# Kernel optimization log

Hardware: AMD Instinct MI355X
Metric: run time of the kernel (lower is better)

The kernel has to match this reference:

```python
import jax, jax.numpy as jnp
import numpy as np

N, C1, C2 = 1024, 384, 128
H, SQK, SV, PQK, PV, OUT = 12, 16, 16, 4, 8, 384
EPS = 1e-8
DOUT = H*SV + 3*H*PV + H*PV + H*C2  # 2112


def setup_inputs():
    key = jax.random.key(0)
    ks = jax.random.split(key, 10)
    inputs_1d = jax.random.normal(ks[0], (N, C1), jnp.float32)
    inputs_2d = jax.random.normal(ks[1], (N, N, C2), jnp.float32)
    mask = jnp.ones((N, 1), jnp.float32)
    # random valid rotations from unit quaternions
    quat = jax.random.normal(ks[2], (N, 4), jnp.float32)
    quat = quat / jnp.linalg.norm(quat, axis=-1, keepdims=True)
    w, x, y, z = quat[:, 0], quat[:, 1], quat[:, 2], quat[:, 3]
    rot = jnp.stack([
        jnp.stack([1 - 2*(y*y + z*z), 2*(x*y - w*z), 2*(x*z + w*y)], -1),
        jnp.stack([2*(x*y + w*z), 1 - 2*(x*x + z*z), 2*(y*z - w*x)], -1),
        jnp.stack([2*(x*z - w*y), 2*(y*z + w*x), 1 - 2*(x*x + y*y)], -1)], -2)
    trans = 10.0 * jax.random.normal(ks[3], (N, 3), jnp.float32)
    s1 = 1.0 / np.sqrt(C1)
    wq = jax.random.normal(ks[4], (C1, H*SQK), jnp.float32) * s1
    bq = jnp.zeros((H*SQK,), jnp.float32)
    wkv = jax.random.normal(ks[5], (C1, H*(SQK + SV)), jnp.float32) * s1
    bkv = jnp.zeros((H*(SQK + SV),), jnp.float32)
    wqp = jax.random.normal(ks[6], (C1, H*3*PQK), jnp.float32) * s1
    bqp = jnp.zeros((H*3*PQK,), jnp.float32)
    wkvp = jax.random.normal(ks[7], (C1, H*3*(PQK + PV)), jnp.float32) * s1
    bkvp = jnp.zeros((H*3*(PQK + PV),), jnp.float32)
    w2d = jax.random.normal(ks[8], (C2, H), jnp.float32) / np.sqrt(C2)
    b2d = jnp.zeros((H,), jnp.float32)
    tpw = jnp.full((H,), np.log(np.e - 1.0), jnp.float32)  # softplus(tpw)=1 at init
    wo = jax.random.normal(ks[9], (DOUT, OUT), jnp.float32) / np.sqrt(DOUT)
    bo = jnp.zeros((OUT,), jnp.float32)
    return dict(inputs_1d=inputs_1d, inputs_2d=inputs_2d, mask=mask, rot=rot, trans=trans,
                wq=wq, bq=bq, wkv=wkv, bkv=bkv, wqp=wqp, bqp=bqp, wkvp=wkvp, bkvp=bkvp,
                w2d=w2d, b2d=b2d, tpw=tpw, wo=wo, bo=bo)


def _ipa(inputs_1d, inputs_2d, mask, rot, trans, wq, bq, wkv, bkv, wqp, bqp,
         wkvp, bkvp, w2d, b2d, tpw, wo, bo):
    n = inputs_1d.shape[0]
    # scalar q/k/v
    q_scalar = (inputs_1d @ wq + bq).reshape(n, H, SQK)
    kv_scalar = (inputs_1d @ wkv + bkv).reshape(n, H, SQK + SV)
    k_scalar, v_scalar = kv_scalar[..., :SQK], kv_scalar[..., SQK:]
    # point q/k/v: local frame -> global frame, x_g = R x_l + t
    q_pl = (inputs_1d @ wqp + bqp).reshape(n, 3, H*PQK)
    q_pg = jnp.einsum('nac,nck->nak', rot, q_pl) + trans[:, :, None]
    q_pt = q_pg.reshape(n, 3, H, PQK).transpose(1, 2, 0, 3)        # (3,H,N,PQK)
    kv_pl = (inputs_1d @ wkvp + bkvp).reshape(n, 3, H*(PQK + PV))
    kv_pg = jnp.einsum('nac,nck->nak', rot, kv_pl) + trans[:, :, None]
    kv_pt = kv_pg.reshape(n, 3, H, PQK + PV).transpose(1, 2, 0, 3)  # (3,H,N,PQK+PV)
    k_pt, v_pt = kv_pt[..., :PQK], kv_pt[..., PQK:]
    # logit weights (3 logit terms)
    scalar_w = np.sqrt(1.0 / (3.0 * SQK))
    point_w = np.sqrt(1.0 / (3.0 * PQK * 9.0 / 2.0)) * jax.nn.softplus(tpw)  # (H,)
    # squared-distance term, expanded to avoid a (3,H,N,N,P) intermediate
    sq = jnp.sum(q_pt * q_pt, axis=(0, 3))                         # (H,N)
    sk = jnp.sum(k_pt * k_pt, axis=(0, 3))                         # (H,N)
    qk = jnp.einsum('chnp,chmp->hnm', q_pt, k_pt)
    dist2 = sq[:, :, None] + sk[:, None, :] - 2.0 * qk             # (H,N,N)
    attn_qk_point = -0.5 * point_w[:, None, None] * dist2
    attn_qk_scalar = jnp.einsum('nhs,mhs->hnm', scalar_w * q_scalar, k_scalar)
    att2d = jnp.transpose(inputs_2d @ w2d + b2d, (2, 0, 1))        # (H,N,N)
    logits = attn_qk_scalar + attn_qk_point + np.sqrt(1.0 / 3.0) * att2d
    mask_2d = mask * jnp.swapaxes(mask, -1, -2)                    # (N,N)
    logits = logits - 1e5 * (1.0 - mask_2d)
    attn = jax.nn.softmax(logits, axis=-1)                         # (H,N,N)
    # aggregate scalar, point and pair outputs with the same weights
    res_scalar = jnp.einsum('hnm,mhs->nhs', attn, v_scalar).reshape(n, H*SV)
    res_pg = jnp.einsum('hnm,chmp->cnhp', attn, v_pt).reshape(3, n, H*PV)
    res_pl = jnp.einsum('nca,cnk->ank', rot, res_pg - trans.T[:, :, None])  # R^T(g-t)
    pt_norm = jnp.sqrt(EPS + jnp.sum(res_pl * res_pl, axis=0))     # (N,H*PV)
    res_2d = jnp.einsum('hnm,nmc->nhc', attn, inputs_2d).reshape(n, H*C2)
    final = jnp.concatenate([res_scalar, res_pl[0], res_pl[1], res_pl[2], pt_norm, res_2d], axis=-1)
    return final @ wo + bo


def reference(inputs_1d, inputs_2d, mask, rot, trans, wq, bq, wkv, bkv, wqp, bqp,
              wkvp, bkvp, w2d, b2d, tpw, wo, bo):
    return _ipa(inputs_1d, inputs_2d, mask, rot, trans, wq, bq, wkv, bkv, wqp, bqp,
                wkvp, bkvp, w2d, b2d, tpw, wo, bo)
```

## Files before the change

kernel.cpp:

```cpp
#include <hip/hip_runtime.h>
#include <math.h>

#define NN_ 1024
#define DOUT_ 2112
#define NOUT_ 384

using f16x8_t = __attribute__((ext_vector_type(8))) _Float16;
using f32x4_t = __attribute__((ext_vector_type(4))) float;

__global__ __launch_bounds__(256) void k_gemm1(
    const float* __restrict__ in1,
    const float* __restrict__ wq, const float* __restrict__ bq,
    const float* __restrict__ wkv, const float* __restrict__ bkv,
    const float* __restrict__ wqp, const float* __restrict__ bqp,
    const float* __restrict__ wkvp, const float* __restrict__ bkvp,
    float* __restrict__ yraw)
{
    __shared__ float a_l[64 * 36];
    __shared__ float b_l[32 * 68];
    const int t = threadIdx.x;
    const int m0 = blockIdx.x * 64, j0 = blockIdx.y * 64;
    const int tx = t & 15, ty = t >> 4;
    float acc[4][4] = {};
    for (int k0 = 0; k0 < 384; k0 += 32) {
        #pragma unroll
        for (int e = 0; e < 2; ++e) {
            int idx = t + 256 * e;
            int r = idx >> 3, c4 = (idx & 7) * 4;
            *(float4*)&a_l[r * 36 + c4] = *(const float4*)&in1[(size_t)(m0 + r) * 384 + k0 + c4];
        }
        #pragma unroll
        for (int e = 0; e < 2; ++e) {
            int idx = t + 256 * e;
            int r = idx >> 4, c4 = (idx & 15) * 4;
            int j = j0 + c4;
            const float* w; int ncol, jj;
            if (j < 192)      { w = wq;   ncol = 192; jj = j; }
            else if (j < 576) { w = wkv;  ncol = 384; jj = j - 192; }
            else if (j < 720) { w = wqp;  ncol = 144; jj = j - 576; }
            else              { w = wkvp; ncol = 432; jj = j - 720; }
            *(float4*)&b_l[r * 68 + c4] = *(const float4*)&w[(size_t)(k0 + r) * ncol + jj];
        }
        __syncthreads();
        #pragma unroll 8
        for (int k = 0; k < 32; ++k) {
            float4 bv = *(const float4*)&b_l[k * 68 + tx * 4];
            #pragma unroll
            for (int i = 0; i < 4; ++i) {
                float av = a_l[(ty * 4 + i) * 36 + k];
                acc[i][0] += av * bv.x; acc[i][1] += av * bv.y;
                acc[i][2] += av * bv.z; acc[i][3] += av * bv.w;
            }
        }
        __syncthreads();
    }
    int j = j0 + tx * 4;
    float4 bias;
    {
        const float* b; int jj;
        if (j < 192)      { b = bq;   jj = j; }
        else if (j < 576) { b = bkv;  jj = j - 192; }
        else if (j < 720) { b = bqp;  jj = j - 576; }
        else              { b = bkvp; jj = j - 720; }
        bias = *(const float4*)&b[jj];
    }
    #pragma unroll
    for (int i = 0; i < 4; ++i) {
        float4 o;
        o.x = acc[i][0] + bias.x; o.y = acc[i][1] + bias.y;
        o.z = acc[i][2] + bias.z; o.w = acc[i][3] + bias.w;
        *(float4*)&yraw[(size_t)(m0 + ty * 4 + i) * 1152 + j] = o;
    }
}

__global__ __launch_bounds__(256) void k_rot(
    const float* __restrict__ yraw, const float* __restrict__ rotm, const float* __restrict__ trans,
    float* __restrict__ qp_arr, float* __restrict__ kpackT4, _Float16* __restrict__ vT,
    float* __restrict__ sq_arr, float* __restrict__ skT)
{
    __shared__ float rt_l[4][12];
    const int t = threadIdx.x;
    const int n0 = blockIdx.x * 4;
    if (t < 48) {
        int n_ = t / 12, i = t % 12;
        rt_l[n_][i] = (i < 9) ? rotm[(n0 + n_) * 9 + i] : trans[(n0 + n_) * 3 + (i - 9)];
    }
    __syncthreads();
    const int n_ = t >> 6, l = t & 63;
    const int n = n0 + n_;
    const float* y = yraw + (size_t)n * 1152;
    const float* R = rt_l[n_];
    #pragma unroll
    for (int jj = 0; jj < 9; ++jj) {
        int o = l + 64 * jj;
        if (o < 144) {
            int a = o / 48, kk = o % 48;
            float v = R[9 + a] + R[a*3+0] * y[576 + kk] + R[a*3+1] * y[576 + 48 + kk] + R[a*3+2] * y[576 + 96 + kk];
            qp_arr[(size_t)n * 144 + o] = v;
        } else if (o < 288) {
            int o2 = o - 144;
            int a = o2 / 48, r2 = o2 % 48;
            int kk = (r2 >> 2) * 12 + (r2 & 3);
            float v = R[9 + a] + R[a*3+0] * y[720 + kk] + R[a*3+1] * y[720 + 144 + kk] + R[a*3+2] * y[720 + 288 + kk];
            int j = 192 + o2;
            kpackT4[(size_t)(j >> 2) * 4096 + 4 * n + (j & 3)] = v;
        } else {
            int o3 = o - 288;
            int a = o3 / 96, r2 = o3 % 96;
            int kk = (r2 >> 3) * 12 + 4 + (r2 & 7);
            float v = R[9 + a] + R[a*3+0] * y[720 + kk] + R[a*3+1] * y[720 + 144 + kk] + R[a*3+2] * y[720 + 288 + kk];
            vT[(size_t)(192 + o3) * 1024 + n] = (_Float16)v;
        }
    }
    #pragma unroll
    for (int jj = 0; jj < 3; ++jj) {
        int o = l + 64 * jj;
        int h = o >> 4, r2 = o & 15;
        kpackT4[(size_t)(o >> 2) * 4096 + 4 * n + (o & 3)] = y[192 + h * 32 + r2];
        vT[(size_t)o * 1024 + n] = (_Float16)y[192 + h * 32 + 16 + r2];
    }
    if (l < 32) vT[(size_t)(480 + l) * 1024 + n] = (_Float16)0.f;
    if (l < 24) {
        int which = l / 12, h = l % 12;
        int base = (which == 0) ? 576 : 720;
        int stride = (which == 0) ? 48 : 144;
        float s = 0.f;
        #pragma unroll
        for (int a = 0; a < 3; ++a) {
            #pragma unroll
            for (int p = 0; p < 4; ++p) {
                int kk = (which == 0) ? (h * 4 + p) : (h * 12 + p);
                float v = R[9 + a] + R[a*3+0] * y[base + kk] + R[a*3+1] * y[base + stride + kk] + R[a*3+2] * y[base + 2 * stride + kk];
                s += v * v;
            }
        }
        if (which == 0) sq_arr[(size_t)n * 12 + h] = s;
        else            skT[(size_t)h * 1024 + n] = s;
    }
}

__global__ __launch_bounds__(256) void k_attn9(
    const float* __restrict__ x2d, const float* __restrict__ mask,
    const float* __restrict__ w2d, const float* __restrict__ b2d, const float* __restrict__ tpw,
    const float* __restrict__ yraw, const float* __restrict__ qp_arr,
    const float* __restrict__ kpackT4, const _Float16* __restrict__ vT,
    const float* __restrict__ sq_arr, const float* __restrict__ skT,
    const float* __restrict__ rotm, const float* __restrict__ trans,
    float* __restrict__ fin)
{
    __shared__ _Float16 x_lT[128][72];
    __shared__ _Float16 tlb[16][72];
    __shared__ _Float16 w2bT[16][136];
    __shared__ float at2_l[64][13];
    __shared__ float qs_l[192], qp_l[144];
    __shared__ float sq_l[12], pw_l[12], b2_l[12];
    __shared__ float rmax_l[12], rsum_l[16], alph_l[16];
    __shared__ float rt_l[12];
    __shared__ float pg_l[288];

    const int t = threadIdx.x;
    const int n = blockIdx.x;

    const int wv = t >> 6, ln = t & 63;
    const int mmS = ln & 15, oS = ln >> 4;
    const int m3 = t & 63, hg = t >> 6;
    const int rowB = (ln >> 4) * 4;

    f32x4_t accM[2] = {{0.f,0.f,0.f,0.f},{0.f,0.f,0.f,0.f}};
    f32x4_t accF[8];
    #pragma unroll
    for (int jt = 0; jt < 8; ++jt) accF[jt] = (f32x4_t){0.f,0.f,0.f,0.f};
    f16x8_t afr[4];

    for (int i = t; i < 2176; i += 256) {
        int h = i / 136, c = i % 136;
        w2bT[h][c] = (h < 12 && c < 128) ? (_Float16)w2d[c * 12 + h] : (_Float16)0.f;
    }
    tlb[12 + (t >> 6)][t & 63] = (_Float16)0.f;
    if (t < 192) qs_l[t] = yraw[(size_t)n * 1152 + t];
    if (t < 144) qp_l[t] = qp_arr[(size_t)n * 144 + t];
    if (t < 12) {
        sq_l[t] = sq_arr[(size_t)n * 12 + t];
        pw_l[t] = 0.13608276348795434f * log1pf(__expf(tpw[t]));
        b2_l[t] = b2d[t];
        rmax_l[t] = -3.0e38f;
        rt_l[t] = (t < 9) ? rotm[n * 9 + t] : trans[n * 3 + (t - 9)];
    }
    if (t < 16) { rsum_l[t] = 0.f; alph_l[t] = 1.0f; }
    const float maskn = mask[n];

    {
        const float* xr = x2d + ((size_t)n * NN_ + wv * 16 + mmS) * 128 + oS * 8;
        #pragma unroll
        for (int kk = 0; kk < 4; ++kk) {
            float4 a = *(const float4*)&xr[kk * 32];
            float4 b = *(const float4*)&xr[kk * 32 + 4];
            f16x8_t f;
            f[0]=(_Float16)a.x; f[1]=(_Float16)a.y; f[2]=(_Float16)a.z; f[3]=(_Float16)a.w;
            f[4]=(_Float16)b.x; f[5]=(_Float16)b.y; f[6]=(_Float16)b.z; f[7]=(_Float16)b.w;
            afr[kk] = f;
        }
    }
    __syncthreads();

    for (int mt = 0; mt < 16; ++mt) {
        const int m0 = mt * 64;
        {
            const int m = wv * 16 + mmS;
            #pragma unroll
            for (int kk = 0; kk < 4; ++kk) {
                const int c0 = kk * 32 + oS * 8;
                #pragma unroll
                for (int i = 0; i < 8; ++i) x_lT[c0 + i][m] = afr[kk][i];
            }
            f32x4_t aA = {0.f, 0.f, 0.f, 0.f};
            #pragma unroll
            for (int kk = 0; kk < 4; ++kk) {
                f16x8_t bfW = *(const f16x8_t*)&w2bT[ln & 15][kk * 32 + (ln >> 4) * 8];
                aA = __builtin_amdgcn_mfma_f32_16x16x32_f16(afr[kk], bfW, aA, 0, 0, 0);
            }
            const int hC = ln & 15;
            if (hC < 12) {
                #pragma unroll
                for (int r = 0; r < 4; ++r)
                    at2_l[wv * 16 + (ln >> 4) * 4 + r][hC] = aA[r];
            }
        }
        __syncthreads();

        {
            int m1 = (mt + 1 == 16) ? 0 : (m0 + 64);
            const float* xr = x2d + ((size_t)n * NN_ + m1 + wv * 16 + mmS) * 128 + oS * 8;
            #pragma unroll
            for (int kk = 0; kk < 4; ++kk) {
                float4 a = *(const float4*)&xr[kk * 32];
                float4 b = *(const float4*)&xr[kk * 32 + 4];
                f16x8_t f;
                f[0]=(_Float16)a.x; f[1]=(_Float16)a.y; f[2]=(_Float16)a.z; f[3]=(_Float16)a.w;
                f[4]=(_Float16)b.x; f[5]=(_Float16)b.y; f[6]=(_Float16)b.z; f[7]=(_Float16)b.w;
                afr[kk] = f;
            }
        }
        {
            const int mg = m0 + m3;
            const float* kb = kpackT4 + 4 * (size_t)mg;
            const float mko = 100000.0f * (1.0f - maskn * mask[mg]);
            #pragma unroll
            for (int e = 0; e < 3; ++e) {
                const int h = hg * 3 + e;
                float4 k0 = *(const float4*)&kb[(size_t)(h * 4 + 0) * 4096];
                float4 k1 = *(const float4*)&kb[(size_t)(h * 4 + 1) * 4096];
                float4 k2 = *(const float4*)&kb[(size_t)(h * 4 + 2) * 4096];
                float4 k3 = *(const float4*)&kb[(size_t)(h * 4 + 3) * 4096];
                float4 p0 = *(const float4*)&kb[(size_t)(48 + h) * 4096];
                float4 p1 = *(const float4*)&kb[(size_t)(60 + h) * 4096];
                float4 p2 = *(const float4*)&kb[(size_t)(72 + h) * 4096];
                float skm = skT[(size_t)h * 1024 + mg];
                const float4* qsn = (const float4*)&qs_l[h * 16];
                float dqs = qsn[0].x*k0.x + qsn[0].y*k0.y + qsn[0].z*k0.z + qsn[0].w*k0.w
                          + qsn[1].x*k1.x + qsn[1].y*k1.y + qsn[1].z*k1.z + qsn[1].w*k1.w
                          + qsn[2].x*k2.x + qsn[2].y*k2.y + qsn[2].z*k2.z + qsn[2].w*k2.w
                          + qsn[3].x*k3.x + qsn[3].y*k3.y + qsn[3].z*k3.z + qsn[3].w*k3.w;
                float4 qA = *(const float4*)&qp_l[h * 4];
                float4 qB = *(const float4*)&qp_l[48 + h * 4];
                float4 qC = *(const float4*)&qp_l[96 + h * 4];
                float qk = qA.x*p0.x + qA.y*p0.y + qA.z*p0.z + qA.w*p0.w
                         + qB.x*p1.x + qB.y*p1.y + qB.z*p1.z + qB.w*p1.w
                         + qC.x*p2.x + qC.y*p2.y + qC.z*p2.z + qC.w*p2.w;
                float pwh = pw_l[h];
                float lg = 0.14433756729740643f * dqs
                         + pwh * qk - 0.5f * pwh * (sq_l[h] + skm)
                         + 0.57735026918962576f * (at2_l[m3][h] + b2_l[h])
                         - mko;
                float tm = lg;
                tm = fmaxf(tm, __shfl_xor(tm, 1));
                tm = fmaxf(tm, __shfl_xor(tm, 2));
                tm = fmaxf(tm, __shfl_xor(tm, 4));
                tm = fmaxf(tm, __shfl_xor(tm, 8));
                tm = fmaxf(tm, __shfl_xor(tm, 16));
                tm = fmaxf(tm, __shfl_xor(tm, 32));
                float om = rmax_l[h];
                float nm = fmaxf(om, tm);
                float p = __expf(lg - nm);
                tlb[h][m3] = (_Float16)p;
                float ps = p;
                ps += __shfl_xor(ps, 1);
                ps += __shfl_xor(ps, 2);
                ps += __shfl_xor(ps, 4);
                ps += __shfl_xor(ps, 8);
                ps += __shfl_xor(ps, 16);
                ps += __shfl_xor(ps, 32);
                if (m3 == 0) {
                    float al = __expf(om - nm);
                    rmax_l[h] = nm;
                    alph_l[h] = al;
                    rsum_l[h] = rsum_l[h] * al + ps;
                }
            }
        }
        __syncthreads();

        {
            f32x4_t av = { alph_l[rowB], alph_l[rowB + 1], alph_l[rowB + 2], alph_l[rowB + 3] };
            accM[0] *= av;
            accM[1] *= av;
            #pragma unroll
            for (int jt = 0; jt < 8; ++jt) accF[jt] *= av;
            f16x8_t pA0 = *(const f16x8_t*)&tlb[ln & 15][(ln >> 4) * 8];
            f16x8_t pA1 = *(const f16x8_t*)&tlb[ln & 15][32 + (ln >> 4) * 8];
            #pragma unroll
            for (int nt = 0; nt < 2; ++nt) {
                int c = wv * 32 + nt * 16 + (ln & 15);
                f16x8_t xB0 = *(const f16x8_t*)&x_lT[c][(ln >> 4) * 8];
                f16x8_t xB1 = *(const f16x8_t*)&x_lT[c][32 + (ln >> 4) * 8];
                accM[nt] = __builtin_amdgcn_mfma_f32_16x16x32_f16(pA0, xB0, accM[nt], 0, 0, 0);
                accM[nt] = __builtin_amdgcn_mfma_f32_16x16x32_f16(pA1, xB1, accM[nt], 0, 0, 0);
            }
            const _Float16* vb = vT + (size_t)m0;
            #pragma unroll
            for (int jt = 0; jt < 8; ++jt) {
                int j = (wv * 8 + jt) * 16 + (ln & 15);
                f16x8_t vB0 = *(const f16x8_t*)&vb[(size_t)j * 1024 + (ln >> 4) * 8];
                f16x8_t vB1 = *(const f16x8_t*)&vb[(size_t)j * 1024 + 32 + (ln >> 4) * 8];
                accF[jt] = __builtin_amdgcn_mfma_f32_16x16x32_f16(pA0, vB0, accF[jt], 0, 0, 0);
                accF[jt] = __builtin_amdgcn_mfma_f32_16x16x32_f16(pA1, vB1, accF[jt], 0, 0, 0);
            }
        }
        __syncthreads();
    }

    #pragma unroll
    for (int nt = 0; nt < 2; ++nt) {
        #pragma unroll
        for (int r = 0; r < 4; ++r) {
            int row = rowB + r;
            if (row < 12) {
                int c = wv * 32 + nt * 16 + (ln & 15);
                fin[(size_t)n * DOUT_ + 576 + (size_t)row * 128 + c] = accM[nt][r] / rsum_l[row];
            }
        }
    }
    #pragma unroll
    for (int jt = 0; jt < 8; ++jt) {
        int j = (wv * 8 + jt) * 16 + (ln & 15);
        if (j < 480) {
            int hj = (j < 192) ? (j >> 4) : (((j - 192) % 96) >> 3);
            if (hj >= rowB && hj < rowB + 4) {
                float val = accF[jt][hj - rowB] / rsum_l[hj];
                if (j < 192) fin[(size_t)n * DOUT_ + j] = val;
                else         pg_l[j - 192] = val;
            }
        }
    }
    __syncthreads();
    if (t < 96) {
        const int k = t;
        float c0 = pg_l[k]       - rt_l[9];
        float c1 = pg_l[96 + k]  - rt_l[10];
        float c2 = pg_l[192 + k] - rt_l[11];
        float r0 = rt_l[0] * c0 + rt_l[3] * c1 + rt_l[6] * c2;
        float r1 = rt_l[1] * c0 + rt_l[4] * c1 + rt_l[7] * c2;
        float r2 = rt_l[2] * c0 + rt_l[5] * c1 + rt_l[8] * c2;
        size_t base = (size_t)n * DOUT_;
        fin[base + 192 + k] = r0;
        fin[base + 288 + k] = r1;
        fin[base + 384 + k] = r2;
        fin[base + 480 + k] = sqrtf(1e-8f + r0 * r0 + r1 * r1 + r2 * r2);
    }
}

__global__ __launch_bounds__(256) void k_out(
    const float* __restrict__ fin, const float* __restrict__ wo,
    float* __restrict__ pout)
{
    __shared__ float a_l[64 * 52];
    __shared__ float b_l[48 * 68];
    const int t = threadIdx.x;
    const int m0 = blockIdx.x * 64, n0 = blockIdx.y * 64, kc = blockIdx.z;
    const int tx = t & 15, ty = t >> 4;
    float acc[4][4] = {};
    for (int k0 = kc * 528; k0 < kc * 528 + 528; k0 += 48) {
        #pragma unroll
        for (int e = 0; e < 3; ++e) {
            int idx = t + 256 * e;
            int r = idx / 12, c4 = (idx % 12) * 4;
            *(float4*)&a_l[r * 52 + c4] = *(const float4*)&fin[(size_t)(m0 + r) * DOUT_ + k0 + c4];
        }
        #pragma unroll
        for (int e = 0; e < 3; ++e) {
            int idx = t + 256 * e;
            int r = idx >> 4, c4 = (idx & 15) * 4;
            *(float4*)&b_l[r * 68 + c4] = *(const float4*)&wo[(size_t)(k0 + r) * 384 + n0 + c4];
        }
        __syncthreads();
        #pragma unroll 4
        for (int k = 0; k < 48; ++k) {
            float4 bv = *(const float4*)&b_l[k * 68 + tx * 4];
            #pragma unroll
            for (int i = 0; i < 4; ++i) {
                float av = a_l[(ty * 4 + i) * 52 + k];
                acc[i][0] += av * bv.x; acc[i][1] += av * bv.y;
                acc[i][2] += av * bv.z; acc[i][3] += av * bv.w;
            }
        }
        __syncthreads();
    }
    float* pr = pout + (size_t)kc * 393216;
    #pragma unroll
    for (int i = 0; i < 4; ++i) {
        float4 o;
        o.x = acc[i][0]; o.y = acc[i][1]; o.z = acc[i][2]; o.w = acc[i][3];
        *(float4*)&pr[(size_t)(m0 + ty * 4 + i) * 384 + n0 + tx * 4] = o;
    }
}

__global__ __launch_bounds__(256) void k_fin(
    const float* __restrict__ pout, const float* __restrict__ bo, float* __restrict__ out)
{
    int idx = blockIdx.x * 256 + threadIdx.x;
    float4 a = *(const float4*)&pout[(size_t)idx * 4];
    float4 b = *(const float4*)&pout[393216 + (size_t)idx * 4];
    float4 c = *(const float4*)&pout[786432 + (size_t)idx * 4];
    float4 d = *(const float4*)&pout[1179648 + (size_t)idx * 4];
    float4 bias = *(const float4*)&bo[(idx % 96) * 4];
    float4 o;
    o.x = a.x + b.x + c.x + d.x + bias.x;
    o.y = a.y + b.y + c.y + d.y + bias.y;
    o.z = a.z + b.z + c.z + d.z + bias.z;
    o.w = a.w + b.w + c.w + d.w + bias.w;
    *(float4*)&out[(size_t)idx * 4] = o;
}

extern "C" void kernel_launch(void* const* d_in, const int* in_sizes, int n_in,
                              void* d_out, int out_size, void* d_ws, size_t ws_size,
                              hipStream_t stream) {
    const float* in1   = (const float*)d_in[0];
    const float* x2d   = (const float*)d_in[1];
    const float* mask  = (const float*)d_in[2];
    const float* rotm  = (const float*)d_in[3];
    const float* trans = (const float*)d_in[4];
    const float* wq    = (const float*)d_in[5];
    const float* bq    = (const float*)d_in[6];
    const float* wkv   = (const float*)d_in[7];
    const float* bkv   = (const float*)d_in[8];
    const float* wqp   = (const float*)d_in[9];
    const float* bqp   = (const float*)d_in[10];
    const float* wkvp  = (const float*)d_in[11];
    const float* bkvp  = (const float*)d_in[12];
    const float* w2d   = (const float*)d_in[13];
    const float* b2d   = (const float*)d_in[14];
    const float* tpw   = (const float*)d_in[15];
    const float* wo    = (const float*)d_in[16];
    const float* bo    = (const float*)d_in[17];
    float* out = (float*)d_out;

    float* ws = (float*)d_ws;
    float* yraw    = ws;
    float* qp_arr  = yraw + 1179648;
    float* kpackT4 = qp_arr + 147456;
    float* vT_f    = kpackT4 + 360448;
    float* sq_arr  = vT_f + 262144;
    float* fin     = sq_arr + 12288;
    float* pout    = fin + 2162688;
    float* skT     = pout + 1572864;
    _Float16* vT = (_Float16*)vT_f;

    hipLaunchKernelGGL(k_gemm1, dim3(16, 18), dim3(256), 0, stream,
        in1, wq, bq, wkv, bkv, wqp, bqp, wkvp, bkvp, yraw);
    hipLaunchKernelGGL(k_rot, dim3(256), dim3(256), 0, stream,
        yraw, rotm, trans, qp_arr, kpackT4, vT, sq_arr, skT);
    hipLaunchKernelGGL(k_attn9, dim3(1024), dim3(256), 0, stream,
        x2d, mask, w2d, b2d, tpw, yraw, qp_arr, kpackT4, vT, sq_arr, skT, rotm, trans, fin);
    hipLaunchKernelGGL(k_out, dim3(16, 6, 4), dim3(256), 0, stream, fin, wo, pout);
    hipLaunchKernelGGL(k_fin, dim3(384), dim3(256), 0, stream, pout, bo, out);
}
```

Measured before the change: 360.5 us.

## Split attention key range across two blocks with flash-style partial merge kernel

The attention kernel now splits the 1024 key positions into two halves via a second grid dimension, so each block processes 512 keys and writes unnormalized partial accumulators plus the running max and sum to a workspace. A new merge kernel combines the two halves with a log-sum-exp rescale, then applies the inverse rotation and the point-norm epilogue. This doubles the number of blocks to raise occupancy and parallelism on the GPU. The cost is an extra kernel launch, extra global traffic for the partials, and a second per-block setup of the shared-memory weight tables.

```diff
diff --git a/kernel.cpp b/kernel.cpp
--- a/kernel.cpp
+++ b/kernel.cpp
@@ -4,6 +4,7 @@
 #define NN_ 1024
 #define DOUT_ 2112
 #define NOUT_ 384
+#define PSTR_ 2040
 
 using f16x8_t = __attribute__((ext_vector_type(8))) _Float16;
 using f32x4_t = __attribute__((ext_vector_type(4))) float;
@@ -139,14 +140,13 @@
     }
 }
 
-__global__ __launch_bounds__(256) void k_attn9(
+__global__ __launch_bounds__(256) void k_attn10(
     const float* __restrict__ x2d, const float* __restrict__ mask,
     const float* __restrict__ w2d, const float* __restrict__ b2d, const float* __restrict__ tpw,
     const float* __restrict__ yraw, const float* __restrict__ qp_arr,
     const float* __restrict__ kpackT4, const _Float16* __restrict__ vT,
     const float* __restrict__ sq_arr, const float* __restrict__ skT,
-    const float* __restrict__ rotm, const float* __restrict__ trans,
-    float* __restrict__ fin)
+    float* __restrict__ part)
 {
     __shared__ _Float16 x_lT[128][72];
     __shared__ _Float16 tlb[16][72];
@@ -155,11 +155,11 @@
     __shared__ float qs_l[192], qp_l[144];
     __shared__ float sq_l[12], pw_l[12], b2_l[12];
     __shared__ float rmax_l[12], rsum_l[16], alph_l[16];
-    __shared__ float rt_l[12];
-    __shared__ float pg_l[288];
 
     const int t = threadIdx.x;
     const int n = blockIdx.x;
+    const int ms = blockIdx.y;
+    const int mbase = ms * 512;
 
     const int wv = t >> 6, ln = t & 63;
     const int mmS = ln & 15, oS = ln >> 4;
@@ -184,13 +184,12 @@
         pw_l[t] = 0.13608276348795434f * log1pf(__expf(tpw[t]));
         b2_l[t] = b2d[t];
         rmax_l[t] = -3.0e38f;
-        rt_l[t] = (t < 9) ? rotm[n * 9 + t] : trans[n * 3 + (t - 9)];
     }
     if (t < 16) { rsum_l[t] = 0.f; alph_l[t] = 1.0f; }
     const float maskn = mask[n];
 
     {
-        const float* xr = x2d + ((size_t)n * NN_ + wv * 16 + mmS) * 128 + oS * 8;
+        const float* xr = x2d + ((size_t)n * NN_ + mbase + wv * 16 + mmS) * 128 + oS * 8;
         #pragma unroll
         for (int kk = 0; kk < 4; ++kk) {
             float4 a = *(const float4*)&xr[kk * 32];
@@ -203,8 +202,8 @@
     }
     __syncthreads();
 
-    for (int mt = 0; mt < 16; ++mt) {
-        const int m0 = mt * 64;
+    for (int mt = 0; mt < 8; ++mt) {
+        const int m0 = mbase + mt * 64;
         {
             const int m = wv * 16 + mmS;
             #pragma unroll
@@ -229,7 +228,7 @@
         __syncthreads();
 
         {
-            int m1 = (mt + 1 == 16) ? 0 : (m0 + 64);
+            int m1 = (mt + 1 == 8) ? mbase : (m0 + 64);
             const float* xr = x2d + ((size_t)n * NN_ + m1 + wv * 16 + mmS) * 128 + oS * 8;
             #pragma unroll
             for (int kk = 0; kk < 4; ++kk) {
@@ -329,6 +328,7 @@
         __syncthreads();
     }
 
+    float* pr = part + ((size_t)ms * NN_ + n) * PSTR_;
     #pragma unroll
     for (int nt = 0; nt < 2; ++nt) {
         #pragma unroll
@@ -336,7 +336,7 @@
             int row = rowB + r;
             if (row < 12) {
                 int c = wv * 32 + nt * 16 + (ln & 15);
-                fin[(size_t)n * DOUT_ + 576 + (size_t)row * 128 + c] = accM[nt][r] / rsum_l[row];
+                pr[(size_t)row * 128 + c] = accM[nt][r];
             }
         }
     }
@@ -345,27 +345,58 @@
         int j = (wv * 8 + jt) * 16 + (ln & 15);
         if (j < 480) {
             int hj = (j < 192) ? (j >> 4) : (((j - 192) % 96) >> 3);
-            if (hj >= rowB && hj < rowB + 4) {
-                float val = accF[jt][hj - rowB] / rsum_l[hj];
-                if (j < 192) fin[(size_t)n * DOUT_ + j] = val;
-                else         pg_l[j - 192] = val;
-            }
-        }
+            if (hj >= rowB && hj < rowB + 4) pr[1536 + j] = accF[jt][hj - rowB];
+        }
+    }
+    if (t < 12) { pr[2016 + t] = rmax_l[t]; pr[2028 + t] = rsum_l[t]; }
+}
+
+__global__ __launch_bounds__(256) void k_merge(
+    const float* __restrict__ part, const float* __restrict__ rotm, const float* __restrict__ trans,
+    float* __restrict__ fin)
+{
+    __shared__ float w0_l[12], w1_l[12], pg_l[288], rt_l[12];
+    const int t = threadIdx.x;
+    const int n = blockIdx.x;
+    const float* p0 = part + (size_t)n * PSTR_;
+    const float* p1 = part + (size_t)(NN_ + n) * PSTR_;
+    if (t < 12) {
+        float m0v = p0[2016 + t], m1v = p1[2016 + t];
+        float gm = fmaxf(m0v, m1v);
+        float f0 = __expf(m0v - gm), f1 = __expf(m1v - gm);
+        float gs = p0[2028 + t] * f0 + p1[2028 + t] * f1;
+        w0_l[t] = f0 / gs; w1_l[t] = f1 / gs;
+    }
+    if (t >= 32 && t < 44) {
+        int i = t - 32;
+        rt_l[i] = (i < 9) ? rotm[n * 9 + i] : trans[n * 3 + i - 9];
+    }
+    __syncthreads();
+    float* fr = fin + (size_t)n * DOUT_;
+    #pragma unroll
+    for (int e = 0; e < 6; ++e) {
+        int idx = t + 256 * e;
+        int h = idx >> 7;
+        fr[576 + idx] = p0[idx] * w0_l[h] + p1[idx] * w1_l[h];
+    }
+    if (t < 240) {
+        int j0 = 2 * t;
+        int h = (j0 < 192) ? (j0 >> 4) : (((j0 - 192) % 96) >> 3);
+        float a0 = p0[1536 + j0] * w0_l[h] + p1[1536 + j0] * w1_l[h];
+        float a1 = p0[1537 + j0] * w0_l[h] + p1[1537 + j0] * w1_l[h];
+        if (j0 < 192) { fr[j0] = a0; fr[j0 + 1] = a1; }
+        else { pg_l[j0 - 192] = a0; pg_l[j0 - 191] = a1; }
     }
     __syncthreads();
     if (t < 96) {
-        const int k = t;
-        float c0 = pg_l[k]       - rt_l[9];
-        float c1 = pg_l[96 + k]  - rt_l[10];
-        float c2 = pg_l[192 + k] - rt_l[11];
+        float c0 = pg_l[t] - rt_l[9];
+        float c1 = pg_l[96 + t] - rt_l[10];
+        float c2 = pg_l[192 + t] - rt_l[11];
         float r0 = rt_l[0] * c0 + rt_l[3] * c1 + rt_l[6] * c2;
         float r1 = rt_l[1] * c0 + rt_l[4] * c1 + rt_l[7] * c2;
         float r2 = rt_l[2] * c0 + rt_l[5] * c1 + rt_l[8] * c2;
-        size_t base = (size_t)n * DOUT_;
-        fin[base + 192 + k] = r0;
-        fin[base + 288 + k] = r1;
-        fin[base + 384 + k] = r2;
-        fin[base + 480 + k] = sqrtf(1e-8f + r0 * r0 + r1 * r1 + r2 * r2);
+        fr[192 + t] = r0; fr[288 + t] = r1; fr[384 + t] = r2;
+        fr[480 + t] = sqrtf(1e-8f + r0 * r0 + r1 * r1 + r2 * r2);
     }
 }
 
@@ -463,14 +494,17 @@
     float* fin     = sq_arr + 12288;
     float* pout    = fin + 2162688;
     float* skT     = pout + 1572864;
+    float* part    = skT + 12288;
     _Float16* vT = (_Float16*)vT_f;
 
     hipLaunchKernelGGL(k_gemm1, dim3(16, 18), dim3(256), 0, stream,
         in1, wq, bq, wkv, bkv, wqp, bqp, wkvp, bkvp, yraw);
     hipLaunchKernelGGL(k_rot, dim3(256), dim3(256), 0, stream,
         yraw, rotm, trans, qp_arr, kpackT4, vT, sq_arr, skT);
-    hipLaunchKernelGGL(k_attn9, dim3(1024), dim3(256), 0, stream,
-        x2d, mask, w2d, b2d, tpw, yraw, qp_arr, kpackT4, vT, sq_arr, skT, rotm, trans, fin);
+    hipLaunchKernelGGL(k_attn10, dim3(1024, 2), dim3(256), 0, stream,
+        x2d, mask, w2d, b2d, tpw, yraw, qp_arr, kpackT4, vT, sq_arr, skT, part);
+    hipLaunchKernelGGL(k_merge, dim3(1024), dim3(256), 0, stream,
+        part, rotm, trans, fin);
     hipLaunchKernelGGL(k_out, dim3(16, 6, 4), dim3(256), 0, stream, fin, wo, pout);
     hipLaunchKernelGGL(k_fin, dim3(384), dim3(256), 0, stream, pout, bo, out);
 }
```

Measured after the change: 567.0 us. +57.3%, slower.
